# Kernel optimization log

Measured on AMD Instinct MI355X. Metric: run time of the kernel, lower is better.

## Reference

```python
import jax, jax.numpy as jnp
import numpy as np

INV_SCALE = 8.0  # math.sqrt(64) in the original source


def setup_inputs() -> dict:
    key = jax.random.key(0)
    kq, kk, kv = jax.random.split(key, 3)
    B, S, D = 8, 2048, 128
    q1 = jax.random.normal(kq, (B, S, D), dtype=jnp.float32)
    k1 = jax.random.normal(kk, (B, S, D), dtype=jnp.float32)
    v1 = jax.random.normal(kv, (B, S, D), dtype=jnp.float32)
    return {"q1": q1, "k1": k1, "v1": v1}


def reference(q1, k1, v1):
    # qk = q1 @ k1^T over last two dims  -> [B, S, S]
    scaled_qk = jnp.einsum("bsd,btd->bst", q1, k1) / INV_SCALE
    # original computes softmax(scaled_qk) but never uses it (dead code);
    # dropout is applied to scaled_qk and is identity in eval mode.
    out = jnp.einsum("bst,btd->bsd", scaled_qk, v1)  # [B, S, D]
    return out
```

## Files before the change

### kernel.cpp

```cpp
#include <hip/hip_runtime.h>
#include <hip/hip_bf16.h>


#define B 8
#define S 2048
#define D 128
#define CH 32
#define SC 64

typedef __attribute__((ext_vector_type(8))) short short8;
typedef __attribute__((ext_vector_type(4))) float f32x4;

static __device__ __forceinline__ short f2bf(float f) {
    __hip_bfloat16 h = __float2bfloat16(f);
    union { __hip_bfloat16 h; short s; } u; u.h = h;
    return u.s;
}
static __device__ __forceinline__ float bf2f(unsigned short s) {
    union { unsigned u; float f; } x; x.u = ((unsigned)s) << 16;
    return x.f;
}

__global__ __launch_bounds__(256) void s1_ktv(
    const float* __restrict__ K, const float* __restrict__ V,
    unsigned short* __restrict__ P)
{
    int blk = blockIdx.x;
    int b = blk >> 6, rem = blk & 63;
    int ch = rem >> 1, h = rem & 1;
    const float* Kb = K + ((size_t)b * S + (size_t)ch * SC) * D;
    const float* Vb = V + ((size_t)b * S + (size_t)ch * SC) * D;

    int tid = threadIdx.x;
    int w = tid >> 6, l = tid & 63;
    int lr = l & 15, lg = l >> 4;
    int dr0 = h * 64 + (w >> 1) * 32;
    int cc0 = (w & 1) * 64;

    f32x4 acc[2][4];
#pragma unroll
    for (int i = 0; i < 2; i++)
#pragma unroll
        for (int j = 0; j < 4; j++) acc[i][j] = (f32x4)0.f;

#pragma unroll
    for (int ks = 0; ks < 2; ++ks) {
        int sb = ks * 32 + lg * 8;
        short8 af[2], bv[4];
#pragma unroll
        for (int fi = 0; fi < 2; ++fi) {
            const float* kp = Kb + (size_t)sb * D + dr0 + fi * 16 + lr;
            float t[8];
#pragma unroll
            for (int i = 0; i < 8; ++i) t[i] = kp[(size_t)i * D];
            short8 s8;
#pragma unroll
            for (int i = 0; i < 8; ++i) s8[i] = f2bf(t[i]);
            af[fi] = s8;
        }
#pragma unroll
        for (int fj = 0; fj < 4; ++fj) {
            const float* vp = Vb + (size_t)sb * D + cc0 + fj * 16 + lr;
            float t[8];
#pragma unroll
            for (int i = 0; i < 8; ++i) t[i] = vp[(size_t)i * D];
            short8 s8;
#pragma unroll
            for (int i = 0; i < 8; ++i) s8[i] = f2bf(t[i]);
            bv[fj] = s8;
        }
#pragma unroll
        for (int fi = 0; fi < 2; ++fi)
#pragma unroll
            for (int fj = 0; fj < 4; ++fj)
                acc[fi][fj] = __builtin_amdgcn_mfma_f32_16x16x32_bf16(
                    af[fi], bv[fj], acc[fi][fj], 0, 0, 0);
    }

    unsigned short* Pb = P + (size_t)(b * CH + ch) * D * D;
#pragma unroll
    for (int fi = 0; fi < 2; ++fi)
#pragma unroll
        for (int fj = 0; fj < 4; ++fj)
#pragma unroll
            for (int j = 0; j < 4; ++j) {
                int row = dr0 + fi * 16 + lg * 4 + j;
                int col = cc0 + fj * 16 + lr;
                Pb[row * D + col] = (unsigned short)f2bf(acc[fi][fj][j]);
            }
}

__global__ __launch_bounds__(256) void s2_reduce(
    const unsigned short* __restrict__ P, unsigned short* __restrict__ MT)
{
    int idx = blockIdx.x * 256 + threadIdx.x;
    int i0 = idx * 2;
    int b = i0 >> 14;
    int r = i0 & 16383;
    const unsigned short* Pb = P + (size_t)(b * CH) * D * D;
    float s0 = 0.f, s1 = 0.f;
#pragma unroll 8
    for (int cc = 0; cc < CH; ++cc) {
        unsigned pair = *(const unsigned*)(Pb + (size_t)cc * D * D + r);
        s0 += bf2f((unsigned short)(pair & 0xFFFF));
        s1 += bf2f((unsigned short)(pair >> 16));
    }
    int d = r >> 7, c = r & 127;
    unsigned short* Mb = MT + (size_t)b * D * D;
    Mb[c * D + d]       = (unsigned short)f2bf(s0 * 0.125f);
    Mb[(c + 1) * D + d] = (unsigned short)f2bf(s1 * 0.125f);
}

__global__ __launch_bounds__(256) void s3_qm(
    const float* __restrict__ Q, const unsigned short* __restrict__ MT,
    float* __restrict__ Out)
{
    int blk = blockIdx.x;
    int b = blk >> 6, t = blk & 63;
    int tid = threadIdx.x;
    int w = tid >> 6, l = tid & 63;
    int lr = l & 15, lg = l >> 4;
    int r0 = t * 32 + (w >> 1) * 16;
    int c0 = (w & 1) * 64;

    const float* Qb = Q + ((size_t)b * S + r0) * D;
    const unsigned short* Mb = MT + (size_t)b * D * D;

    f32x4 acc[4];
#pragma unroll
    for (int j = 0; j < 4; j++) acc[j] = (f32x4)0.f;

#pragma unroll
    for (int ks = 0; ks < 4; ++ks) {
        int k0 = ks * 32 + lg * 8;
        const float* qp = Qb + (size_t)lr * D + k0;
        float4 q0 = *(const float4*)qp;
        float4 q1 = *(const float4*)(qp + 4);
        short8 a;
        a[0] = f2bf(q0.x); a[1] = f2bf(q0.y); a[2] = f2bf(q0.z); a[3] = f2bf(q0.w);
        a[4] = f2bf(q1.x); a[5] = f2bf(q1.y); a[6] = f2bf(q1.z); a[7] = f2bf(q1.w);
#pragma unroll
        for (int fj = 0; fj < 4; ++fj) {
            short8 bb = *(const short8*)(Mb + (size_t)(c0 + fj * 16 + lr) * D + k0);
            acc[fj] = __builtin_amdgcn_mfma_f32_16x16x32_bf16(a, bb, acc[fj], 0, 0, 0);
        }
    }

    float* Ob = Out + ((size_t)b * S + r0) * D;
#pragma unroll
    for (int fj = 0; fj < 4; ++fj)
#pragma unroll
        for (int j = 0; j < 4; ++j)
            Ob[(size_t)(lg * 4 + j) * D + c0 + fj * 16 + lr] = acc[fj][j];
}

extern "C" void kernel_launch(void* const* d_in, const int* in_sizes, int n_in,
                              void* d_out, int out_size, void* d_ws, size_t ws_size,
                              hipStream_t stream)
{
    const float* q = (const float*)d_in[0];
    const float* k = (const float*)d_in[1];
    const float* v = (const float*)d_in[2];
    float* out = (float*)d_out;

    unsigned short* P  = (unsigned short*)d_ws;
    unsigned short* MT = P + (size_t)B * CH * D * D;

    s1_ktv<<<B * CH * 2, 256, 0, stream>>>(k, v, P);
    s2_reduce<<<(B * D * D / 2) / 256, 256, 0, stream>>>(P, MT);
    s3_qm<<<B * 64, 256, 0, stream>>>(q, MT, out);
}
```

Before: 24.37 us.

## Fuse partial-sum reduction into Q·M kernel and enlarge K^T V chunks

The K^T·V stage now covers 8 chunks of 256 rows with 512-thread blocks instead of 32 chunks of 64 rows, giving four times fewer partial matrices to write and reduce. The separate reduce kernel is removed. Each Q·M block now sums the 8 bf16 partials itself, transposes the result into swizzled shared memory and runs the MFMA from LDS over 64 rows. This drops one launch and the global round trip of the reduced matrix. In exchange, every Q·M block redundantly re-reduces 8×128×128 partials, and stage 1 launches only 128 blocks, so parallelism is lower.

```diff
diff --git a/kernel.cpp b/kernel.cpp
--- a/kernel.cpp
+++ b/kernel.cpp
@@ -5,8 +5,8 @@
 #define B 8
 #define S 2048
 #define D 128
-#define CH 32
-#define SC 64
+#define CH 8
+#define SC 256
 
 typedef __attribute__((ext_vector_type(8))) short short8;
 typedef __attribute__((ext_vector_type(4))) float f32x4;
@@ -21,12 +21,12 @@
     return x.f;
 }
 
-__global__ __launch_bounds__(256) void s1_ktv(
+__global__ __launch_bounds__(512) void k1_ktv(
     const float* __restrict__ K, const float* __restrict__ V,
     unsigned short* __restrict__ P)
 {
     int blk = blockIdx.x;
-    int b = blk >> 6, rem = blk & 63;
+    int b = blk >> 4, rem = blk & 15;
     int ch = rem >> 1, h = rem & 1;
     const float* Kb = K + ((size_t)b * S + (size_t)ch * SC) * D;
     const float* Vb = V + ((size_t)b * S + (size_t)ch * SC) * D;
@@ -34,19 +34,18 @@
     int tid = threadIdx.x;
     int w = tid >> 6, l = tid & 63;
     int lr = l & 15, lg = l >> 4;
-    int dr0 = h * 64 + (w >> 1) * 32;
-    int cc0 = (w & 1) * 64;
+    int dr0 = h * 64 + (w >> 2) * 32;
+    int cc0 = (w & 3) * 32;
 
-    f32x4 acc[2][4];
+    f32x4 acc[2][2];
 #pragma unroll
     for (int i = 0; i < 2; i++)
 #pragma unroll
-        for (int j = 0; j < 4; j++) acc[i][j] = (f32x4)0.f;
+        for (int j = 0; j < 2; j++) acc[i][j] = (f32x4)0.f;
 
-#pragma unroll
-    for (int ks = 0; ks < 2; ++ks) {
+    for (int ks = 0; ks < 8; ++ks) {
         int sb = ks * 32 + lg * 8;
-        short8 af[2], bv[4];
+        short8 af[2], bv[2];
 #pragma unroll
         for (int fi = 0; fi < 2; ++fi) {
             const float* kp = Kb + (size_t)sb * D + dr0 + fi * 16 + lr;
@@ -59,7 +58,7 @@
             af[fi] = s8;
         }
 #pragma unroll
-        for (int fj = 0; fj < 4; ++fj) {
+        for (int fj = 0; fj < 2; ++fj) {
             const float* vp = Vb + (size_t)sb * D + cc0 + fj * 16 + lr;
             float t[8];
 #pragma unroll
@@ -72,7 +71,7 @@
 #pragma unroll
         for (int fi = 0; fi < 2; ++fi)
 #pragma unroll
-            for (int fj = 0; fj < 4; ++fj)
+            for (int fj = 0; fj < 2; ++fj)
                 acc[fi][fj] = __builtin_amdgcn_mfma_f32_16x16x32_bf16(
                     af[fi], bv[fj], acc[fi][fj], 0, 0, 0);
     }
@@ -81,7 +80,7 @@
 #pragma unroll
     for (int fi = 0; fi < 2; ++fi)
 #pragma unroll
-        for (int fj = 0; fj < 4; ++fj)
+        for (int fj = 0; fj < 2; ++fj)
 #pragma unroll
             for (int j = 0; j < 4; ++j) {
                 int row = dr0 + fi * 16 + lg * 4 + j;
@@ -90,45 +89,59 @@
             }
 }
 
-__global__ __launch_bounds__(256) void s2_reduce(
-    const unsigned short* __restrict__ P, unsigned short* __restrict__ MT)
-{
-    int idx = blockIdx.x * 256 + threadIdx.x;
-    int i0 = idx * 2;
-    int b = i0 >> 14;
-    int r = i0 & 16383;
-    const unsigned short* Pb = P + (size_t)(b * CH) * D * D;
-    float s0 = 0.f, s1 = 0.f;
-#pragma unroll 8
-    for (int cc = 0; cc < CH; ++cc) {
-        unsigned pair = *(const unsigned*)(Pb + (size_t)cc * D * D + r);
-        s0 += bf2f((unsigned short)(pair & 0xFFFF));
-        s1 += bf2f((unsigned short)(pair >> 16));
-    }
-    int d = r >> 7, c = r & 127;
-    unsigned short* Mb = MT + (size_t)b * D * D;
-    Mb[c * D + d]       = (unsigned short)f2bf(s0 * 0.125f);
-    Mb[(c + 1) * D + d] = (unsigned short)f2bf(s1 * 0.125f);
-}
-
-__global__ __launch_bounds__(256) void s3_qm(
-    const float* __restrict__ Q, const unsigned short* __restrict__ MT,
+__global__ __launch_bounds__(256) void k2_rqm(
+    const float* __restrict__ Q, const unsigned short* __restrict__ P,
     float* __restrict__ Out)
 {
+    __shared__ unsigned short MT[D * D];
+
     int blk = blockIdx.x;
-    int b = blk >> 6, t = blk & 63;
+    int b = blk >> 5, t = blk & 31;
     int tid = threadIdx.x;
+
+    int cblk = tid & 15, dblk = tid >> 4;
+    int c0 = cblk * 8, d0 = dblk * 8;
+    const unsigned short* Pb = P + (size_t)(b * CH) * D * D;
+
+    float m[8][8];
+#pragma unroll
+    for (int j = 0; j < 8; ++j)
+#pragma unroll
+        for (int i = 0; i < 8; ++i) m[j][i] = 0.f;
+
+#pragma unroll
+    for (int cc = 0; cc < CH; ++cc) {
+#pragma unroll
+        for (int j = 0; j < 8; ++j) {
+            short8 pv = *(const short8*)(Pb + (size_t)cc * D * D + (d0 + j) * D + c0);
+#pragma unroll
+            for (int i = 0; i < 8; ++i)
+                m[j][i] += bf2f((unsigned short)pv[i]);
+        }
+    }
+
+    char* mt = (char*)MT;
+#pragma unroll
+    for (int i = 0; i < 8; ++i) {
+        int c = c0 + i;
+        short8 sv;
+#pragma unroll
+        for (int j = 0; j < 8; ++j) sv[j] = f2bf(m[j][i] * 0.125f);
+        int X = ((c & 7) ^ (cblk & 7)) & 7;
+        int byte = (c * 256 + 2 * d0) ^ (X << 4);
+        *(short8*)(mt + byte) = sv;
+    }
+    __syncthreads();
+
     int w = tid >> 6, l = tid & 63;
     int lr = l & 15, lg = l >> 4;
-    int r0 = t * 32 + (w >> 1) * 16;
-    int c0 = (w & 1) * 64;
+    int r0 = t * 64 + w * 16;
 
     const float* Qb = Q + ((size_t)b * S + r0) * D;
-    const unsigned short* Mb = MT + (size_t)b * D * D;
 
-    f32x4 acc[4];
+    f32x4 acc[8];
 #pragma unroll
-    for (int j = 0; j < 4; j++) acc[j] = (f32x4)0.f;
+    for (int j = 0; j < 8; ++j) acc[j] = (f32x4)0.f;
 
 #pragma unroll
     for (int ks = 0; ks < 4; ++ks) {
@@ -140,18 +153,21 @@
         a[0] = f2bf(q0.x); a[1] = f2bf(q0.y); a[2] = f2bf(q0.z); a[3] = f2bf(q0.w);
         a[4] = f2bf(q1.x); a[5] = f2bf(q1.y); a[6] = f2bf(q1.z); a[7] = f2bf(q1.w);
 #pragma unroll
-        for (int fj = 0; fj < 4; ++fj) {
-            short8 bb = *(const short8*)(Mb + (size_t)(c0 + fj * 16 + lr) * D + k0);
+        for (int fj = 0; fj < 8; ++fj) {
+            int c = fj * 16 + lr;
+            int X = ((c & 7) ^ ((c >> 3) & 7)) & 7;
+            int byte = (c * 256 + 2 * k0) ^ (X << 4);
+            short8 bb = *(const short8*)(mt + byte);
             acc[fj] = __builtin_amdgcn_mfma_f32_16x16x32_bf16(a, bb, acc[fj], 0, 0, 0);
         }
     }
 
     float* Ob = Out + ((size_t)b * S + r0) * D;
 #pragma unroll
-    for (int fj = 0; fj < 4; ++fj)
+    for (int fj = 0; fj < 8; ++fj)
 #pragma unroll
         for (int j = 0; j < 4; ++j)
-            Ob[(size_t)(lg * 4 + j) * D + c0 + fj * 16 + lr] = acc[fj][j];
+            Ob[(size_t)(lg * 4 + j) * D + fj * 16 + lr] = acc[fj][j];
 }
 
 extern "C" void kernel_launch(void* const* d_in, const int* in_sizes, int n_in,
@@ -163,10 +179,8 @@
     const float* v = (const float*)d_in[2];
     float* out = (float*)d_out;
 
-    unsigned short* P  = (unsigned short*)d_ws;
-    unsigned short* MT = P + (size_t)B * CH * D * D;
+    unsigned short* P = (unsigned short*)d_ws;
 
-    s1_ktv<<<B * CH * 2, 256, 0, stream>>>(k, v, P);
-    s2_reduce<<<(B * D * D / 2) / 256, 256, 0, stream>>>(P, MT);
-    s3_qm<<<B * 64, 256, 0, stream>>>(q, MT, out);
+    k1_ktv<<<B * CH * 2, 512, 0, stream>>>(k, v, P);
+    k2_rqm<<<B * 32, 256, 0, stream>>>(q, P, out);
 }
```

Result: faster. 23.75 us (-2.6%).
